# Performance work log

Hardware: AMD Instinct MI355X
Metric: run time of the kernel (lower is better)

The kernel has to match this reference:

```python
import jax, jax.numpy as jnp
import numpy as np

COMMITMENT_COST = 0.25
K, D = 1024, 64          # num_embeddings, embedding_dim
B, T = 32, 4096          # batch, tokens per batch element


def setup_inputs() -> dict:
    key = jax.random.key(0)
    k1, k2 = jax.random.split(key)
    inputs = jax.random.normal(k1, (B, T, D), dtype=jnp.float32)
    # xavier_uniform over [K, D]: bound = sqrt(6/(K+D))
    bound = float(np.sqrt(6.0 / (K + D)))
    embedding = jax.random.uniform(k2, (K, D), dtype=jnp.float32,
                                   minval=-bound, maxval=bound)
    return {"inputs": inputs, "embedding": embedding}


def reference(inputs, embedding):
    input_shape = inputs.shape
    flat = inputs.reshape(-1, embedding.shape[1])            # [N, D]
    input_sq = jnp.sum(flat ** 2, axis=1, keepdims=True)     # [N, 1]
    embed_sq = jnp.sum(embedding ** 2, axis=1)               # [K]
    dot = flat @ embedding.T                                 # [N, K]
    distances = input_sq + embed_sq - 2.0 * dot              # [N, K]
    idx = jnp.argmin(distances, axis=1)                      # [N]
    quant = embedding[idx]                                   # [N, D]
    q_latent_loss = jnp.mean((quant - jax.lax.stop_gradient(flat)) ** 2)
    e_latent_loss = jnp.mean((jax.lax.stop_gradient(quant) - flat) ** 2)
    loss = q_latent_loss + COMMITMENT_COST * e_latent_loss
    # straight-through estimator
    quant_st = flat + jax.lax.stop_gradient(quant - flat)
    quant_st = quant_st.reshape(input_shape)
    encoding_indices = idx.reshape(input_shape[0], -1)
    return quant_st, loss, encoding_indices
```

## Files before the change

### kernel.cpp

```cpp
#include <hip/hip_runtime.h>


#define KC 1024
#define DD 64
#define NTOK (32 * 4096)
#define QUANT_ELEMS ((size_t)NTOK * DD)
#define LOSS_OFF QUANT_ELEMS
#define IDX_OFF (QUANT_ELEMS + 1)

#define WS_E2 0
#define WS_X2 2048
#define WS_PACKED_F (2048 + NTOK)
#define WS_BFRAG_F (WS_PACKED_F + 2 * NTOK)
#define WS_BSUM (WS_BFRAG_F + 65536)

#define COMBINE_BLOCKS (NTOK / 64)

typedef _Float16 f16x8 __attribute__((ext_vector_type(8)));
typedef float f32x4 __attribute__((ext_vector_type(4)));

__device__ __forceinline__ unsigned int sortable_bits(float f) {
  unsigned int b = __float_as_uint(f);
  return b ^ (unsigned int)(((int)b >> 31) | 0x80000000);
}

__device__ __forceinline__ float row_sumsq_np8(const float* p) {
  float r[8];
#pragma unroll
  for (int j = 0; j < 8; ++j) r[j] = p[j] * p[j];
#pragma unroll
  for (int i = 1; i < 8; ++i)
#pragma unroll
    for (int j = 0; j < 8; ++j) {
      float v = p[i * 8 + j];
      r[j] += v * v;
    }
  return ((r[0] + r[1]) + (r[2] + r[3])) + ((r[4] + r[5]) + (r[6] + r[7]));
}

__global__ void vq_setup(const float* __restrict__ x_in,
                         const float* __restrict__ emb,
                         float* __restrict__ ws) {
  const int b = blockIdx.x;
  const int tid = threadIdx.x;
  if (b < 512) {
    const int t = b * 256 + tid;
    ws[WS_X2 + t] = row_sumsq_np8(x_in + (size_t)t * DD);
  } else if (b < 576) {
    const int nt = b - 512;
    const int f = tid >> 6;
    const int lane = tid & 63;
    const int plane = f >> 1, ks = f & 1;
    const int n = nt * 16 + (lane & 15);
    const int kb = ks * 32 + ((lane >> 4) & 3) * 8;
    const float* ep = emb + (size_t)n * DD + kb;
    f16x8 o;
#pragma unroll
    for (int j = 0; j < 8; ++j) {
      float v = ep[j];
      _Float16 h = (_Float16)v;
      o[j] = (plane == 0) ? h : (_Float16)(v - (float)h);
    }
    ((f16x8*)(ws + WS_BFRAG_F))[(nt * 4 + f) * 64 + lane] = o;
  } else {
    const int k = (b - 576) * 256 + tid;
    ws[WS_E2 + k] = row_sumsq_np8(emb + (size_t)k * DD);
  }
}

__launch_bounds__(256, 2)
__global__ void vq_dist_mfma(const float* __restrict__ x_in,
                             const float* __restrict__ ws_ro,
                             unsigned long long* __restrict__ packed) {
  const int tid = threadIdx.x;
  const int wave = tid >> 6, lane = tid & 63;
  const int quad = lane >> 4, l16 = lane & 15;
  const int tokBase = blockIdx.x * 128 + wave * 32;

  __shared__ float4 Bf[2][1024];
  __shared__ float E2s[KC];

  const float4* bsrc = (const float4*)(ws_ro + WS_BFRAG_F);

  float4 st[4];
#pragma unroll
  for (int i = 0; i < 4; ++i) st[i] = bsrc[i * 256 + tid];
#pragma unroll
  for (int i = 0; i < 4; ++i)
    E2s[i * 256 + tid] = ws_ro[WS_E2 + i * 256 + tid];

  f16x8 ah[2][2], al[2][2];
#pragma unroll
  for (int ms = 0; ms < 2; ++ms) {
    const float* xr = x_in + (size_t)(tokBase + ms * 16 + l16) * DD;
#pragma unroll
    for (int ks = 0; ks < 2; ++ks) {
      const float4* p = (const float4*)(xr + ks * 32 + quad * 8);
      float4 v0 = p[0], v1 = p[1];
      float vv[8] = {v0.x, v0.y, v0.z, v0.w, v1.x, v1.y, v1.z, v1.w};
#pragma unroll
      for (int j = 0; j < 8; ++j) {
        _Float16 h = (_Float16)vv[j];
        ah[ms][ks][j] = h;
        al[ms][ks][j] = (_Float16)(vv[j] - (float)h);
      }
    }
  }

  float x2v[2][4];
#pragma unroll
  for (int ms = 0; ms < 2; ++ms)
#pragma unroll
    for (int r = 0; r < 4; ++r)
      x2v[ms][r] = ws_ro[WS_X2 + tokBase + ms * 16 + quad * 4 + r];

#pragma unroll
  for (int i = 0; i < 4; ++i) Bf[0][i * 256 + tid] = st[i];

  float best[2][4];
  int bidx[2][4];
#pragma unroll
  for (int ms = 0; ms < 2; ++ms)
#pragma unroll
    for (int r = 0; r < 4; ++r) { best[ms][r] = 3.402823466e38f; bidx[ms][r] = 0; }

  __syncthreads();

  for (int q = 0; q < 16; ++q) {
    const int buf = q & 1;
    if (q < 15) {
#pragma unroll
      for (int i = 0; i < 4; ++i)
        st[i] = bsrc[(q + 1) * 1024 + i * 256 + tid];
    }
    const f16x8* bfp = (const f16x8*)Bf[buf];
#pragma unroll
    for (int lt = 0; lt < 4; ++lt) {
      const int ch = lt * 4;
      f16x8 bh0 = bfp[(ch + 0) * 64 + lane];
      f16x8 bh1 = bfp[(ch + 1) * 64 + lane];
      f16x8 bl0 = bfp[(ch + 2) * 64 + lane];
      f16x8 bl1 = bfp[(ch + 3) * 64 + lane];
      const int ncur = q * 64 + lt * 16 + l16;
      const float e2v = E2s[ncur];
      f32x4 acc[2];
#pragma unroll
      for (int ms = 0; ms < 2; ++ms) acc[ms] = (f32x4){0.f, 0.f, 0.f, 0.f};
#pragma unroll
      for (int ms = 0; ms < 2; ++ms)
        acc[ms] = __builtin_amdgcn_mfma_f32_16x16x32_f16(ah[ms][0], bh0, acc[ms], 0, 0, 0);
#pragma unroll
      for (int ms = 0; ms < 2; ++ms)
        acc[ms] = __builtin_amdgcn_mfma_f32_16x16x32_f16(ah[ms][1], bh1, acc[ms], 0, 0, 0);
#pragma unroll
      for (int ms = 0; ms < 2; ++ms)
        acc[ms] = __builtin_amdgcn_mfma_f32_16x16x32_f16(al[ms][0], bh0, acc[ms], 0, 0, 0);
#pragma unroll
      for (int ms = 0; ms < 2; ++ms)
        acc[ms] = __builtin_amdgcn_mfma_f32_16x16x32_f16(al[ms][1], bh1, acc[ms], 0, 0, 0);
#pragma unroll
      for (int ms = 0; ms < 2; ++ms)
        acc[ms] = __builtin_amdgcn_mfma_f32_16x16x32_f16(ah[ms][0], bl0, acc[ms], 0, 0, 0);
#pragma unroll
      for (int ms = 0; ms < 2; ++ms)
        acc[ms] = __builtin_amdgcn_mfma_f32_16x16x32_f16(ah[ms][1], bl1, acc[ms], 0, 0, 0);
#pragma unroll
      for (int ms = 0; ms < 2; ++ms)
#pragma unroll
        for (int r = 0; r < 4; ++r) {
          float s = __builtin_fmaf(-2.0f, acc[ms][r], x2v[ms][r] + e2v);
          if (s < best[ms][r]) { best[ms][r] = s; bidx[ms][r] = ncur; }
        }
    }
    if (q < 15) {
#pragma unroll
      for (int i = 0; i < 4; ++i) Bf[buf ^ 1][i * 256 + tid] = st[i];
    }
    __syncthreads();
  }

#pragma unroll
  for (int ms = 0; ms < 2; ++ms)
#pragma unroll
    for (int r = 0; r < 4; ++r) {
      unsigned long long key =
          ((unsigned long long)sortable_bits(best[ms][r]) << 32) |
          (unsigned int)bidx[ms][r];
#pragma unroll
      for (int m = 1; m < 16; m <<= 1) {
        unsigned long long o = __shfl_xor(key, m);
        key = o < key ? o : key;
      }
      if (l16 == 0)
        packed[tokBase + ms * 16 + quad * 4 + r] = key;
    }
}

__global__ void vq_combine(const float* __restrict__ emb,
                           const unsigned long long* __restrict__ packed,
                           float* __restrict__ out,
                           float* __restrict__ blocksum) {
  const int tid = threadIdx.x;
  const int token = blockIdx.x * 64 + (tid >> 2);
  const int part = tid & 3;

  const unsigned long long key = packed[token];
  const int bidx = (int)(unsigned int)key;

  float err = 0.0f;
  if (part == 0) {
    out[IDX_OFF + (size_t)token] = (float)bidx;
    unsigned int u = (unsigned int)(key >> 32);
    unsigned int fb = (u & 0x80000000u) ? (u ^ 0x80000000u) : ~u;
    err = __uint_as_float(fb);
  }

  const float4* eq = (const float4*)(emb + (size_t)bidx * DD) + part * 4;
  float4* op = (float4*)(out + (size_t)token * DD) + part * 4;
  float4 v0 = eq[0], v1 = eq[1], v2 = eq[2], v3 = eq[3];
  op[0] = v0; op[1] = v1; op[2] = v2; op[3] = v3;

#pragma unroll
  for (int off = 32; off > 0; off >>= 1) err += __shfl_down(err, off);
  __shared__ float wsum[4];
  const int wid = tid >> 6;
  if ((tid & 63) == 0) wsum[wid] = err;
  __syncthreads();
  if (tid == 0)
    blocksum[blockIdx.x] = (wsum[0] + wsum[1]) + (wsum[2] + wsum[3]);
}

__global__ void vq_finish(const float* __restrict__ blocksum,
                          float* __restrict__ out) {
  const int tid = threadIdx.x;
  float s = 0.0f;
#pragma unroll
  for (int i = 0; i < COMBINE_BLOCKS / 256; ++i)
    s += blocksum[i * 256 + tid];
#pragma unroll
  for (int off = 32; off > 0; off >>= 1) s += __shfl_down(s, off);
  __shared__ float wsum[4];
  const int wid = tid >> 6;
  if ((tid & 63) == 0) wsum[wid] = s;
  __syncthreads();
  if (tid == 0) {
    float total = (wsum[0] + wsum[1]) + (wsum[2] + wsum[3]);
    float m = total / (float)QUANT_ELEMS;
    out[LOSS_OFF] = m + 0.25f * m;
  }
}

extern "C" void kernel_launch(void* const* d_in, const int* in_sizes, int n_in,
                              void* d_out, int out_size, void* d_ws, size_t ws_size,
                              hipStream_t stream) {
  const float* x = (const float*)d_in[0];
  const float* emb = (const float*)d_in[1];
  float* out = (float*)d_out;
  float* ws = (float*)d_ws;
  unsigned long long* packed = (unsigned long long*)(ws + WS_PACKED_F);

  vq_setup<<<580, 256, 0, stream>>>(x, emb, ws);
  vq_dist_mfma<<<NTOK / 128, 256, 0, stream>>>(x, ws, packed);
  vq_combine<<<COMBINE_BLOCKS, 256, 0, stream>>>(emb, packed, out, ws + WS_BSUM);
  vq_finish<<<1, 256, 0, stream>>>(ws + WS_BSUM, out);
}
```

Measured before the change: 153.5 us.

## Fuse input norm and gather/loss epilogue into the MFMA distance kernel

Per-token squared norms are now computed inside the distance kernel through shared memory, replacing a separate pass over the input in the setup kernel. The argmin gather, index write and loss partial sums move into the distance kernel's epilogue, removing the combine kernel and the packed-key workspace round trip. This cuts one launch and one full extra read of the 32 MB input. The cost is extra serial work in the distance kernel's prologue and epilogue, plus an uncoalesced per-row norm load by half of each wave.

Measured after the change: 139.4 us. 1.1x faster.

```diff
diff --git a/kernel.cpp b/kernel.cpp
--- a/kernel.cpp
+++ b/kernel.cpp
@@ -9,12 +9,10 @@
 #define IDX_OFF (QUANT_ELEMS + 1)
 
 #define WS_E2 0
-#define WS_X2 2048
-#define WS_PACKED_F (2048 + NTOK)
-#define WS_BFRAG_F (WS_PACKED_F + 2 * NTOK)
+#define WS_BFRAG_F 2048
 #define WS_BSUM (WS_BFRAG_F + 65536)
 
-#define COMBINE_BLOCKS (NTOK / 64)
+#define DIST_BLOCKS (NTOK / 128)
 
 typedef _Float16 f16x8 __attribute__((ext_vector_type(8)));
 typedef float f32x4 __attribute__((ext_vector_type(4)));
@@ -24,6 +22,11 @@
   return b ^ (unsigned int)(((int)b >> 31) | 0x80000000);
 }
 
+__device__ __forceinline__ float unsortable_bits(unsigned int u) {
+  unsigned int fb = (u & 0x80000000u) ? (u ^ 0x80000000u) : ~u;
+  return __uint_as_float(fb);
+}
+
 __device__ __forceinline__ float row_sumsq_np8(const float* p) {
   float r[8];
 #pragma unroll
@@ -38,16 +41,12 @@
   return ((r[0] + r[1]) + (r[2] + r[3])) + ((r[4] + r[5]) + (r[6] + r[7]));
 }
 
-__global__ void vq_setup(const float* __restrict__ x_in,
-                         const float* __restrict__ emb,
+__global__ void vq_setup(const float* __restrict__ emb,
                          float* __restrict__ ws) {
   const int b = blockIdx.x;
   const int tid = threadIdx.x;
-  if (b < 512) {
-    const int t = b * 256 + tid;
-    ws[WS_X2 + t] = row_sumsq_np8(x_in + (size_t)t * DD);
-  } else if (b < 576) {
-    const int nt = b - 512;
+  if (b < 64) {
+    const int nt = b;
     const int f = tid >> 6;
     const int lane = tid & 63;
     const int plane = f >> 1, ks = f & 1;
@@ -63,15 +62,17 @@
     }
     ((f16x8*)(ws + WS_BFRAG_F))[(nt * 4 + f) * 64 + lane] = o;
   } else {
-    const int k = (b - 576) * 256 + tid;
+    const int k = (b - 64) * 256 + tid;
     ws[WS_E2 + k] = row_sumsq_np8(emb + (size_t)k * DD);
   }
 }
 
 __launch_bounds__(256, 2)
 __global__ void vq_dist_mfma(const float* __restrict__ x_in,
+                             const float* __restrict__ emb,
                              const float* __restrict__ ws_ro,
-                             unsigned long long* __restrict__ packed) {
+                             float* __restrict__ out,
+                             float* __restrict__ blocksum) {
   const int tid = threadIdx.x;
   const int wave = tid >> 6, lane = tid & 63;
   const int quad = lane >> 4, l16 = lane & 15;
@@ -79,6 +80,8 @@
 
   __shared__ float4 Bf[2][1024];
   __shared__ float E2s[KC];
+  __shared__ float x2s[128];
+  __shared__ float wsum[4];
 
   const float4* bsrc = (const float4*)(ws_ro + WS_BFRAG_F);
 
@@ -88,6 +91,10 @@
 #pragma unroll
   for (int i = 0; i < 4; ++i)
     E2s[i * 256 + tid] = ws_ro[WS_E2 + i * 256 + tid];
+
+  if (lane < 32)
+    x2s[wave * 32 + lane] =
+        row_sumsq_np8(x_in + (size_t)(tokBase + lane) * DD);
 
   f16x8 ah[2][2], al[2][2];
 #pragma unroll
@@ -107,13 +114,6 @@
     }
   }
 
-  float x2v[2][4];
-#pragma unroll
-  for (int ms = 0; ms < 2; ++ms)
-#pragma unroll
-    for (int r = 0; r < 4; ++r)
-      x2v[ms][r] = ws_ro[WS_X2 + tokBase + ms * 16 + quad * 4 + r];
-
 #pragma unroll
   for (int i = 0; i < 4; ++i) Bf[0][i * 256 + tid] = st[i];
 
@@ -125,6 +125,13 @@
     for (int r = 0; r < 4; ++r) { best[ms][r] = 3.402823466e38f; bidx[ms][r] = 0; }
 
   __syncthreads();
+
+  float x2v[2][4];
+#pragma unroll
+  for (int ms = 0; ms < 2; ++ms)
+#pragma unroll
+    for (int r = 0; r < 4; ++r)
+      x2v[ms][r] = x2s[wave * 32 + ms * 16 + quad * 4 + r];
 
   for (int q = 0; q < 16; ++q) {
     const int buf = q & 1;
@@ -179,52 +186,38 @@
     __syncthreads();
   }
 
+  unsigned long long key[2][4];
 #pragma unroll
   for (int ms = 0; ms < 2; ++ms)
 #pragma unroll
     for (int r = 0; r < 4; ++r) {
-      unsigned long long key =
+      unsigned long long k =
           ((unsigned long long)sortable_bits(best[ms][r]) << 32) |
           (unsigned int)bidx[ms][r];
 #pragma unroll
       for (int m = 1; m < 16; m <<= 1) {
-        unsigned long long o = __shfl_xor(key, m);
-        key = o < key ? o : key;
+        unsigned long long o = __shfl_xor(k, m);
+        k = o < k ? o : k;
       }
-      if (l16 == 0)
-        packed[tokBase + ms * 16 + quad * 4 + r] = key;
-    }
-}
-
-__global__ void vq_combine(const float* __restrict__ emb,
-                           const unsigned long long* __restrict__ packed,
-                           float* __restrict__ out,
-                           float* __restrict__ blocksum) {
-  const int tid = threadIdx.x;
-  const int token = blockIdx.x * 64 + (tid >> 2);
-  const int part = tid & 3;
-
-  const unsigned long long key = packed[token];
-  const int bidx = (int)(unsigned int)key;
-
-  float err = 0.0f;
-  if (part == 0) {
-    out[IDX_OFF + (size_t)token] = (float)bidx;
-    unsigned int u = (unsigned int)(key >> 32);
-    unsigned int fb = (u & 0x80000000u) ? (u ^ 0x80000000u) : ~u;
-    err = __uint_as_float(fb);
-  }
-
-  const float4* eq = (const float4*)(emb + (size_t)bidx * DD) + part * 4;
-  float4* op = (float4*)(out + (size_t)token * DD) + part * 4;
-  float4 v0 = eq[0], v1 = eq[1], v2 = eq[2], v3 = eq[3];
-  op[0] = v0; op[1] = v1; op[2] = v2; op[3] = v3;
-
-#pragma unroll
-  for (int off = 32; off > 0; off >>= 1) err += __shfl_down(err, off);
-  __shared__ float wsum[4];
-  const int wid = tid >> 6;
-  if ((tid & 63) == 0) wsum[wid] = err;
+      key[ms][r] = k;
+    }
+
+  float qsum = 0.0f;
+#pragma unroll
+  for (int ms = 0; ms < 2; ++ms)
+#pragma unroll
+    for (int r = 0; r < 4; ++r) {
+      const int token = tokBase + ms * 16 + quad * 4 + r;
+      const int widx = (int)(unsigned int)key[ms][r];
+      if (l16 == 0) out[IDX_OFF + (size_t)token] = (float)widx;
+      const float4 v = ((const float4*)(emb + (size_t)widx * DD))[l16];
+      ((float4*)(out + (size_t)token * DD))[l16] = v;
+      qsum += unsortable_bits((unsigned int)(key[ms][r] >> 32));
+    }
+
+  float tot = __shfl(qsum, 0) + __shfl(qsum, 16) +
+              __shfl(qsum, 32) + __shfl(qsum, 48);
+  if (lane == 0) wsum[wave] = tot;
   __syncthreads();
   if (tid == 0)
     blocksum[blockIdx.x] = (wsum[0] + wsum[1]) + (wsum[2] + wsum[3]);
@@ -235,7 +228,7 @@
   const int tid = threadIdx.x;
   float s = 0.0f;
 #pragma unroll
-  for (int i = 0; i < COMBINE_BLOCKS / 256; ++i)
+  for (int i = 0; i < DIST_BLOCKS / 256; ++i)
     s += blocksum[i * 256 + tid];
 #pragma unroll
   for (int off = 32; off > 0; off >>= 1) s += __shfl_down(s, off);
@@ -257,10 +250,8 @@
   const float* emb = (const float*)d_in[1];
   float* out = (float*)d_out;
   float* ws = (float*)d_ws;
-  unsigned long long* packed = (unsigned long long*)(ws + WS_PACKED_F);
-
-  vq_setup<<<580, 256, 0, stream>>>(x, emb, ws);
-  vq_dist_mfma<<<NTOK / 128, 256, 0, stream>>>(x, ws, packed);
-  vq_combine<<<COMBINE_BLOCKS, 256, 0, stream>>>(emb, packed, out, ws + WS_BSUM);
+
+  vq_setup<<<68, 256, 0, stream>>>(emb, ws);
+  vq_dist_mfma<<<DIST_BLOCKS, 256, 0, stream>>>(x, emb, ws, out, ws + WS_BSUM);
   vq_finish<<<1, 256, 0, stream>>>(ws + WS_BSUM, out);
 }
```
